# Optimization experiments

Hardware: AMD Instinct MI355X
Metric: run time of the kernel (lower is better)

## Reference

```python
import jax, jax.numpy as jnp
import numpy as np

BETA = 0.9  # WalkLayer beta


def setup_inputs() -> dict:
    key = jax.random.key(0)
    k1, k2, k3 = jax.random.split(key, 3)
    B, N, K = 2, 64, 64
    graph = jax.random.normal(k1, (B, N, N, K), dtype=jnp.float32)
    W = jax.random.normal(k2, (K, K), dtype=jnp.float32)
    mask_ = jax.random.randint(k3, (B, N, N, N), 0, 2).astype(bool)
    return {"graph": graph, "W": W, "mask_": mask_}


def reference(graph, W, mask_):
    # WalkLayer.forward with activate='relu'
    B, N, _, K = graph.shape
    # generate: project then outer-product walk expansion
    g1 = jnp.einsum('bijk,kl->bijl', graph, W)            # [B,N,N,K]
    g5 = jnp.einsum('bijk,bjmk->bijmk', g1, graph)        # [B,N,N,N,K]
    # mask_invalid_paths_o: zero all diagonals (j==m, i==j, i==m)
    eye = jnp.eye(N, dtype=bool)
    diag = (eye[None, None, :, :, None]   # j==m
            | eye[None, :, :, None, None]  # i==j
            | eye[None, :, None, :, None])  # i==m
    g5 = jnp.where(diag, 0.0, g5)
    g5 = jnp.where(mask_[..., None], g5, 0.0)
    # where(all-zero over k, 0, g5): no-op numerically, kept for fidelity
    g5 = jnp.where(jnp.all(g5 == 0.0, axis=4, keepdims=True), 0.0, g5)
    # aggregate_relu
    beta_mat = jnp.where(jnp.all(g5 == 0.0, axis=2), 1.0, BETA)  # [B,N,N,K]
    new = jnp.sum(jax.nn.relu(g5), axis=2)                        # [B,N,N,K]
    # torch.lerp(new, old, beta_mat) = new + beta_mat * (old - new)
    return new + beta_mat * (graph - new)
```

## Files before the change

kernel.cpp:

```cpp
#include <hip/hip_runtime.h>

#define NN 64
#define KK 64
#define BETA_C 0.9f

__global__ __launch_bounds__(1024, 4) void walk_fused1(const float* __restrict__ graph,
                                                       const float* __restrict__ W,
                                                       const int* __restrict__ mask,
                                                       float* __restrict__ out) {
    __shared__ float Ws[KK][KK];
    __shared__ float g1s[NN][KK];
    __shared__ int   ms[NN][33];

    int bid = blockIdx.x;
    int b, i, mh;
    if (gridDim.x == 256) {
        int xcdsel = bid & 7;
        b  = xcdsel >> 2;
        mh = (xcdsel >> 1) & 1;
        i  = ((xcdsel & 1) << 5) | (bid >> 3);
    } else {
        mh = bid & 1;
        i  = (bid >> 1) & 63;
        b  = bid >> 7;
    }

    int t    = threadIdx.x;
    int lane = t & 63;
    int w    = __builtin_amdgcn_readfirstlane(t >> 6);

    size_t biBase = (size_t)(b * NN + i);

    ((float4*)&Ws[0][0])[t] = ((const float4*)W)[t];

    {
        const int* mbase = mask + (biBase * NN) * NN + mh * 32;
        int j = t >> 5, c = t & 31;
        ms[j][c]      = mbase[(size_t)j * NN + c];
        ms[j + 32][c] = mbase[(size_t)(j + 32) * NN + c];
    }
    __syncthreads();

    if (w < 8) {
        int r0 = w * 8;
        const float4* a = (const float4*)(graph + (biBase * NN + r0) * KK);
        float acc[8] = {0.f, 0.f, 0.f, 0.f, 0.f, 0.f, 0.f, 0.f};
#pragma unroll
        for (int k4 = 0; k4 < 16; ++k4) {
            float4 x[8];
#pragma unroll
            for (int r = 0; r < 8; ++r) x[r] = a[k4 + 16 * r];
            float w0 = Ws[4 * k4 + 0][lane];
            float w1 = Ws[4 * k4 + 1][lane];
            float w2 = Ws[4 * k4 + 2][lane];
            float w3 = Ws[4 * k4 + 3][lane];
#pragma unroll
            for (int r = 0; r < 8; ++r) {
                acc[r] = fmaf(x[r].x, w0, acc[r]);
                acc[r] = fmaf(x[r].y, w1, acc[r]);
                acc[r] = fmaf(x[r].z, w2, acc[r]);
                acc[r] = fmaf(x[r].w, w3, acc[r]);
            }
        }
#pragma unroll
        for (int r = 0; r < 8; ++r) g1s[r0 + r][lane] = acc[r];
    }
    __syncthreads();

    int m0 = mh * 32 + 2 * w;
    int m1 = m0 + 1;

    bool v0 = (ms[lane][2 * w + 0] != 0) & (lane != m0) & (lane != i);
    bool v1 = (ms[lane][2 * w + 1] != 0) & (lane != m1) & (lane != i);
    unsigned long long vm0 = __ballot(v0);
    unsigned long long vm1 = __ballot(v1);
    if (i == m0) vm0 = 0ULL;
    if (i == m1) vm1 = 0ULL;
    unsigned long long vmU = vm0 | vm1;

    const float* gb0 = graph + ((size_t)b * NN * NN + m0) * KK;
    const float* gb1 = graph + ((size_t)b * NN * NN + m1) * KK;

    float a0 = 0.f, s0 = 0.f, a1 = 0.f, s1 = 0.f;
    while (vmU) {
        unsigned long long tv = vmU;
        int  jj[8];
        bool lv[8];
#pragma unroll
        for (int n = 0; n < 8; ++n) {
            lv[n] = (tv != 0ULL);
            jj[n] = (int)__builtin_ctzll(lv[n] ? tv : 1ULL);
            tv &= tv - 1ULL;
        }
        vmU = tv;
        float gv0[8], gv1[8], gw[8];
#pragma unroll
        for (int n = 0; n < 8; ++n) {
            gv0[n] = gb0[(size_t)jj[n] * (NN * KK) + lane];
            gv1[n] = gb1[(size_t)jj[n] * (NN * KK) + lane];
            gw[n]  = g1s[jj[n]][lane];
        }
#pragma unroll
        for (int n = 0; n < 8; ++n) {
            bool c0 = lv[n] && (((vm0 >> jj[n]) & 1ULL) != 0ULL);
            bool c1 = lv[n] && (((vm1 >> jj[n]) & 1ULL) != 0ULL);
            float p0 = c0 ? gv0[n] * gw[n] : 0.f;
            float p1 = c1 ? gv1[n] * gw[n] : 0.f;
            a0 += p0; s0 += fabsf(p0);
            a1 += p1; s1 += fabsf(p1);
        }
    }

    {
        size_t o0 = (biBase * NN + m0) * KK + lane;
        size_t o1 = (biBase * NN + m1) * KK + lane;
        float old0 = graph[o0];
        float old1 = graph[o1];
        float nw0 = (a0 + s0) * 0.5f;
        float nw1 = (a1 + s1) * 0.5f;
        float be0 = (s0 != 0.f) ? BETA_C : 1.0f;
        float be1 = (s1 != 0.f) ? BETA_C : 1.0f;
        out[o0] = nw0 + be0 * (old0 - nw0);
        out[o1] = nw1 + be1 * (old1 - nw1);
    }
}

extern "C" void kernel_launch(void* const* d_in, const int* in_sizes, int n_in,
                              void* d_out, int out_size, void* d_ws, size_t ws_size,
                              hipStream_t stream) {
    const float* graph = (const float*)d_in[0];
    const float* W     = (const float*)d_in[1];
    const int*   mask  = (const int*)d_in[2];
    float*       out   = (float*)d_out;

    int B = in_sizes[0] / (NN * NN * KK);
    walk_fused1<<<B * NN * 2, 1024, 0, stream>>>(graph, W, mask, out);
}
```

Before: 19.01 us.

## Split wave lanes across two m columns and prefetch gathers before the projection

```diff
diff --git a/kernel.cpp b/kernel.cpp
--- a/kernel.cpp
+++ b/kernel.cpp
@@ -4,7 +4,7 @@
 #define KK 64
 #define BETA_C 0.9f
 
-__global__ __launch_bounds__(1024, 4) void walk_fused1(const float* __restrict__ graph,
+__global__ __launch_bounds__(1024, 4) void walk_fused2(const float* __restrict__ graph,
                                                        const float* __restrict__ W,
                                                        const int* __restrict__ mask,
                                                        float* __restrict__ out) {
@@ -41,6 +41,43 @@
     }
     __syncthreads();
 
+    int m0 = mh * 32 + 2 * w;
+    int m1 = m0 + 1;
+    bool v0 = (ms[lane][2 * w + 0] != 0) & (lane != m0) & (lane != i);
+    bool v1 = (ms[lane][2 * w + 1] != 0) & (lane != m1) & (lane != i);
+    unsigned long long vm0 = __ballot(v0);
+    unsigned long long vm1 = __ballot(v1);
+    if (i == m0) vm0 = 0ULL;
+    if (i == m1) vm1 = 0ULL;
+
+    int half = lane >> 5;
+    int kp   = lane & 31;
+    int mlane = half ? m1 : m0;
+    int vbase = mlane * 32 + kp;
+
+    const float2* gb2 = (const float2*)(graph + (size_t)b * NN * NN * KK);
+    const float2* g1p = (const float2*)&g1s[0][0];
+
+    auto extract_issue = [&](int* jvv, bool* kll, float2* gvv) {
+#pragma unroll
+        for (int n = 0; n < 8; ++n) {
+            bool l0n = (vm0 != 0ULL);
+            int  j0  = (int)__builtin_ctzll(l0n ? vm0 : 1ULL);
+            vm0 &= vm0 - 1ULL;
+            bool l1n = (vm1 != 0ULL);
+            int  j1  = (int)__builtin_ctzll(l1n ? vm1 : 1ULL);
+            vm1 &= vm1 - 1ULL;
+            int j   = half ? j1 : j0;
+            kll[n]  = half ? l1n : l0n;
+            jvv[n]  = j;
+            gvv[n]  = gb2[(size_t)j * (NN * KK / 2) + vbase];
+        }
+    };
+
+    float2 gvA[8]; int jvA[8]; bool klA[8];
+    bool haveA = ((vm0 | vm1) != 0ULL);
+    if (haveA) extract_issue(jvA, klA, gvA);
+
     if (w < 8) {
         int r0 = w * 8;
         const float4* a = (const float4*)(graph + (biBase * NN + r0) * KK);
@@ -67,61 +104,35 @@
     }
     __syncthreads();
 
-    int m0 = mh * 32 + 2 * w;
-    int m1 = m0 + 1;
-
-    bool v0 = (ms[lane][2 * w + 0] != 0) & (lane != m0) & (lane != i);
-    bool v1 = (ms[lane][2 * w + 1] != 0) & (lane != m1) & (lane != i);
-    unsigned long long vm0 = __ballot(v0);
-    unsigned long long vm1 = __ballot(v1);
-    if (i == m0) vm0 = 0ULL;
-    if (i == m1) vm1 = 0ULL;
-    unsigned long long vmU = vm0 | vm1;
-
-    const float* gb0 = graph + ((size_t)b * NN * NN + m0) * KK;
-    const float* gb1 = graph + ((size_t)b * NN * NN + m1) * KK;
-
-    float a0 = 0.f, s0 = 0.f, a1 = 0.f, s1 = 0.f;
-    while (vmU) {
-        unsigned long long tv = vmU;
-        int  jj[8];
-        bool lv[8];
+    float accx = 0.f, absx = 0.f, accy = 0.f, absy = 0.f;
+    while (haveA) {
+        bool haveB = ((vm0 | vm1) != 0ULL);
+        float2 gvB[8]; int jvB[8]; bool klB[8];
+        if (haveB) extract_issue(jvB, klB, gvB);
 #pragma unroll
         for (int n = 0; n < 8; ++n) {
-            lv[n] = (tv != 0ULL);
-            jj[n] = (int)__builtin_ctzll(lv[n] ? tv : 1ULL);
-            tv &= tv - 1ULL;
+            float2 gw = g1p[jvA[n] * (KK / 2) + kp];
+            float px = klA[n] ? gvA[n].x * gw.x : 0.f;
+            float py = klA[n] ? gvA[n].y * gw.y : 0.f;
+            accx += px; absx += fabsf(px);
+            accy += py; absy += fabsf(py);
         }
-        vmU = tv;
-        float gv0[8], gv1[8], gw[8];
+        haveA = haveB;
 #pragma unroll
-        for (int n = 0; n < 8; ++n) {
-            gv0[n] = gb0[(size_t)jj[n] * (NN * KK) + lane];
-            gv1[n] = gb1[(size_t)jj[n] * (NN * KK) + lane];
-            gw[n]  = g1s[jj[n]][lane];
-        }
-#pragma unroll
-        for (int n = 0; n < 8; ++n) {
-            bool c0 = lv[n] && (((vm0 >> jj[n]) & 1ULL) != 0ULL);
-            bool c1 = lv[n] && (((vm1 >> jj[n]) & 1ULL) != 0ULL);
-            float p0 = c0 ? gv0[n] * gw[n] : 0.f;
-            float p1 = c1 ? gv1[n] * gw[n] : 0.f;
-            a0 += p0; s0 += fabsf(p0);
-            a1 += p1; s1 += fabsf(p1);
-        }
+        for (int n = 0; n < 8; ++n) { gvA[n] = gvB[n]; jvA[n] = jvB[n]; klA[n] = klB[n]; }
     }
 
     {
-        size_t o0 = (biBase * NN + m0) * KK + lane;
-        size_t o1 = (biBase * NN + m1) * KK + lane;
-        float old0 = graph[o0];
-        float old1 = graph[o1];
-        float nw0 = (a0 + s0) * 0.5f;
-        float nw1 = (a1 + s1) * 0.5f;
-        float be0 = (s0 != 0.f) ? BETA_C : 1.0f;
-        float be1 = (s1 != 0.f) ? BETA_C : 1.0f;
-        out[o0] = nw0 + be0 * (old0 - nw0);
-        out[o1] = nw1 + be1 * (old1 - nw1);
+        size_t o2 = (biBase * NN + mlane) * (KK / 2) + kp;
+        float2 old = ((const float2*)graph)[o2];
+        float nwx = (accx + absx) * 0.5f;
+        float nwy = (accy + absy) * 0.5f;
+        float bx = (absx != 0.f) ? BETA_C : 1.0f;
+        float by = (absy != 0.f) ? BETA_C : 1.0f;
+        float2 res;
+        res.x = nwx + bx * (old.x - nwx);
+        res.y = nwy + by * (old.y - nwy);
+        ((float2*)out)[o2] = res;
     }
 }
 
@@ -134,5 +145,5 @@
     float*       out   = (float*)d_out;
 
     int B = in_sizes[0] / (NN * NN * KK);
-    walk_fused1<<<B * NN * 2, 1024, 0, stream>>>(graph, W, mask, out);
+    walk_fused2<<<B * NN * 2, 1024, 0, stream>>>(graph, W, mask, out);
 }
```

New measurement: 19.48 us. 1.02x slower.

## Split work into quarter blocks and software-pipeline walk gathers ahead of projection

Applied to the files above, without the earlier changes.

```diff
diff --git a/kernel.cpp b/kernel.cpp
--- a/kernel.cpp
+++ b/kernel.cpp
@@ -4,26 +4,20 @@
 #define KK 64
 #define BETA_C 0.9f
 
-__global__ __launch_bounds__(1024, 4) void walk_fused1(const float* __restrict__ graph,
-                                                       const float* __restrict__ W,
-                                                       const int* __restrict__ mask,
-                                                       float* __restrict__ out) {
+__global__ __launch_bounds__(512, 4) void walk_fused3(const float* __restrict__ graph,
+                                                      const float* __restrict__ W,
+                                                      const int* __restrict__ mask,
+                                                      float* __restrict__ out) {
     __shared__ float Ws[KK][KK];
     __shared__ float g1s[NN][KK];
-    __shared__ int   ms[NN][33];
+    __shared__ int   ms[NN][17];
 
     int bid = blockIdx.x;
-    int b, i, mh;
-    if (gridDim.x == 256) {
-        int xcdsel = bid & 7;
-        b  = xcdsel >> 2;
-        mh = (xcdsel >> 1) & 1;
-        i  = ((xcdsel & 1) << 5) | (bid >> 3);
-    } else {
-        mh = bid & 1;
-        i  = (bid >> 1) & 63;
-        b  = bid >> 7;
-    }
+    int q  = bid & 3;
+    int Bc = gridDim.x >> 8;
+    int r  = bid >> 2;
+    int b  = (Bc == 2) ? (r & 1) : (r % Bc);
+    int i  = (Bc == 2) ? (r >> 1) : (r / Bc);
 
     int t    = threadIdx.x;
     int lane = t & 63;
@@ -31,17 +25,71 @@
 
     size_t biBase = (size_t)(b * NN + i);
 
-    ((float4*)&Ws[0][0])[t] = ((const float4*)W)[t];
-
     {
-        const int* mbase = mask + (biBase * NN) * NN + mh * 32;
-        int j = t >> 5, c = t & 31;
-        ms[j][c]      = mbase[(size_t)j * NN + c];
-        ms[j + 32][c] = mbase[(size_t)(j + 32) * NN + c];
+        float4* wd = (float4*)&Ws[0][0];
+        const float4* wsrc = (const float4*)W;
+        wd[t]       = wsrc[t];
+        wd[t + 512] = wsrc[t + 512];
+    }
+    {
+        const int* mbase = mask + (biBase * NN) * NN + q * 16;
+        int j0 = t >> 4, c0 = t & 15;
+        ms[j0][c0]      = mbase[(size_t)j0 * NN + c0];
+        ms[j0 + 32][c0] = mbase[(size_t)(j0 + 32) * NN + c0];
     }
     __syncthreads();
 
-    if (w < 8) {
+    int m0 = q * 16 + 2 * w;
+    int m1 = m0 + 1;
+    bool v0 = (ms[lane][2 * w + 0] != 0) & (lane != m0) & (lane != i);
+    bool v1 = (ms[lane][2 * w + 1] != 0) & (lane != m1) & (lane != i);
+    unsigned long long vm0 = __ballot(v0);
+    unsigned long long vm1 = __ballot(v1);
+    if (i == m0) vm0 = 0ULL;
+    if (i == m1) vm1 = 0ULL;
+
+    const float* gm0 = graph + ((size_t)b * NN * NN + m0) * KK;
+    const float* gm1 = graph + ((size_t)b * NN * NN + m1) * KK;
+
+    int  jA0[8], jA1[8], jB0[8], jB1[8];
+    bool lA0[8], lA1[8], lB0[8], lB1[8];
+    float gvA0[8], gvA1[8], gvB0[8], gvB1[8];
+
+    auto extract = [&](int* j0a, int* j1a, bool* l0a, bool* l1a,
+                       float* gv0, float* gv1) {
+#pragma unroll
+        for (int n = 0; n < 8; ++n) {
+            l0a[n] = (vm0 != 0ULL);
+            j0a[n] = (int)__builtin_ctzll(l0a[n] ? vm0 : 1ULL);
+            vm0 &= vm0 - 1ULL;
+            l1a[n] = (vm1 != 0ULL);
+            j1a[n] = (int)__builtin_ctzll(l1a[n] ? vm1 : 1ULL);
+            vm1 &= vm1 - 1ULL;
+            gv0[n] = gm0[(size_t)j0a[n] * (NN * KK) + lane];
+            gv1[n] = gm1[(size_t)j1a[n] * (NN * KK) + lane];
+        }
+    };
+
+    float ac0 = 0.f, ab0 = 0.f, ac1 = 0.f, ab1 = 0.f;
+    auto consume = [&](int* j0a, int* j1a, bool* l0a, bool* l1a,
+                       float* gv0, float* gv1) {
+#pragma unroll
+        for (int n = 0; n < 8; ++n) {
+            float w0v = g1s[j0a[n]][lane];
+            float w1v = g1s[j1a[n]][lane];
+            float p0 = l0a[n] ? gv0[n] * w0v : 0.f;
+            float p1 = l1a[n] ? gv1[n] * w1v : 0.f;
+            ac0 += p0; ab0 += fabsf(p0);
+            ac1 += p1; ab1 += fabsf(p1);
+        }
+    };
+
+    bool haveA = ((vm0 | vm1) != 0ULL);
+    if (haveA) extract(jA0, jA1, lA0, lA1, gvA0, gvA1);
+    float old0 = gm0[(size_t)i * (NN * KK) + lane];
+    float old1 = gm1[(size_t)i * (NN * KK) + lane];
+
+    {
         int r0 = w * 8;
         const float4* a = (const float4*)(graph + (biBase * NN + r0) * KK);
         float acc[8] = {0.f, 0.f, 0.f, 0.f, 0.f, 0.f, 0.f, 0.f};
@@ -49,77 +97,41 @@
         for (int k4 = 0; k4 < 16; ++k4) {
             float4 x[8];
 #pragma unroll
-            for (int r = 0; r < 8; ++r) x[r] = a[k4 + 16 * r];
+            for (int rr = 0; rr < 8; ++rr) x[rr] = a[k4 + 16 * rr];
             float w0 = Ws[4 * k4 + 0][lane];
             float w1 = Ws[4 * k4 + 1][lane];
             float w2 = Ws[4 * k4 + 2][lane];
             float w3 = Ws[4 * k4 + 3][lane];
 #pragma unroll
-            for (int r = 0; r < 8; ++r) {
-                acc[r] = fmaf(x[r].x, w0, acc[r]);
-                acc[r] = fmaf(x[r].y, w1, acc[r]);
-                acc[r] = fmaf(x[r].z, w2, acc[r]);
-                acc[r] = fmaf(x[r].w, w3, acc[r]);
+            for (int rr = 0; rr < 8; ++rr) {
+                acc[rr] = fmaf(x[rr].x, w0, acc[rr]);
+                acc[rr] = fmaf(x[rr].y, w1, acc[rr]);
+                acc[rr] = fmaf(x[rr].z, w2, acc[rr]);
+                acc[rr] = fmaf(x[rr].w, w3, acc[rr]);
             }
         }
 #pragma unroll
-        for (int r = 0; r < 8; ++r) g1s[r0 + r][lane] = acc[r];
+        for (int rr = 0; rr < 8; ++rr) g1s[r0 + rr][lane] = acc[rr];
     }
     __syncthreads();
 
-    int m0 = mh * 32 + 2 * w;
-    int m1 = m0 + 1;
-
-    bool v0 = (ms[lane][2 * w + 0] != 0) & (lane != m0) & (lane != i);
-    bool v1 = (ms[lane][2 * w + 1] != 0) & (lane != m1) & (lane != i);
-    unsigned long long vm0 = __ballot(v0);
-    unsigned long long vm1 = __ballot(v1);
-    if (i == m0) vm0 = 0ULL;
-    if (i == m1) vm1 = 0ULL;
-    unsigned long long vmU = vm0 | vm1;
-
-    const float* gb0 = graph + ((size_t)b * NN * NN + m0) * KK;
-    const float* gb1 = graph + ((size_t)b * NN * NN + m1) * KK;
-
-    float a0 = 0.f, s0 = 0.f, a1 = 0.f, s1 = 0.f;
-    while (vmU) {
-        unsigned long long tv = vmU;
-        int  jj[8];
-        bool lv[8];
-#pragma unroll
-        for (int n = 0; n < 8; ++n) {
-            lv[n] = (tv != 0ULL);
-            jj[n] = (int)__builtin_ctzll(lv[n] ? tv : 1ULL);
-            tv &= tv - 1ULL;
-        }
-        vmU = tv;
-        float gv0[8], gv1[8], gw[8];
-#pragma unroll
-        for (int n = 0; n < 8; ++n) {
-            gv0[n] = gb0[(size_t)jj[n] * (NN * KK) + lane];
-            gv1[n] = gb1[(size_t)jj[n] * (NN * KK) + lane];
-            gw[n]  = g1s[jj[n]][lane];
-        }
-#pragma unroll
-        for (int n = 0; n < 8; ++n) {
-            bool c0 = lv[n] && (((vm0 >> jj[n]) & 1ULL) != 0ULL);
-            bool c1 = lv[n] && (((vm1 >> jj[n]) & 1ULL) != 0ULL);
-            float p0 = c0 ? gv0[n] * gw[n] : 0.f;
-            float p1 = c1 ? gv1[n] * gw[n] : 0.f;
-            a0 += p0; s0 += fabsf(p0);
-            a1 += p1; s1 += fabsf(p1);
-        }
+    while (haveA) {
+        bool haveB = ((vm0 | vm1) != 0ULL);
+        if (haveB) extract(jB0, jB1, lB0, lB1, gvB0, gvB1);
+        consume(jA0, jA1, lA0, lA1, gvA0, gvA1);
+        if (!haveB) break;
+        haveA = ((vm0 | vm1) != 0ULL);
+        if (haveA) extract(jA0, jA1, lA0, lA1, gvA0, gvA1);
+        consume(jB0, jB1, lB0, lB1, gvB0, gvB1);
     }
 
     {
         size_t o0 = (biBase * NN + m0) * KK + lane;
         size_t o1 = (biBase * NN + m1) * KK + lane;
-        float old0 = graph[o0];
-        float old1 = graph[o1];
-        float nw0 = (a0 + s0) * 0.5f;
-        float nw1 = (a1 + s1) * 0.5f;
-        float be0 = (s0 != 0.f) ? BETA_C : 1.0f;
-        float be1 = (s1 != 0.f) ? BETA_C : 1.0f;
+        float nw0 = (ac0 + ab0) * 0.5f;
+        float nw1 = (ac1 + ab1) * 0.5f;
+        float be0 = (ab0 != 0.f) ? BETA_C : 1.0f;
+        float be1 = (ab1 != 0.f) ? BETA_C : 1.0f;
         out[o0] = nw0 + be0 * (old0 - nw0);
         out[o1] = nw1 + be1 * (old1 - nw1);
     }
@@ -134,5 +146,5 @@
     float*       out   = (float*)d_out;
 
     int B = in_sizes[0] / (NN * NN * KK);
-    walk_fused1<<<B * NN * 2, 1024, 0, stream>>>(graph, W, mask, out);
+    walk_fused3<<<B * NN * 4, 512, 0, stream>>>(graph, W, mask, out);
 }
```

Result: slower. 20.92 us (+10.1%).
